# Performance work log

Hardware: AMD Instinct MI355X
Metric: run time of the kernel (lower is better)

Reference implementation:

```python
import jax, jax.numpy as jnp
import numpy as np

THR = 1.0
ALPHA = 5.0
C = 0.4
TAU_U = 20.0
DT = 1.0

def slayer(x):
    # SE-adlif SLAYER surrogate: c*alpha / (2*exp(alpha*|x|))
    return C * ALPHA / (2.0 * jnp.exp(jnp.abs(x) * ALPHA))

def setup_inputs() -> dict:
    key = jax.random.key(0)
    k1, k2, k3 = jax.random.split(key, 3)
    B, T, IN, OUT = 64, 1000, 512, 512
    x = jax.random.normal(k1, (B, T, IN), dtype=jnp.float32)
    lim = 1.0 / np.sqrt(IN)
    weight = jax.random.uniform(k2, (OUT, IN), minval=-lim, maxval=lim, dtype=jnp.float32)
    bias = jnp.zeros((OUT,), jnp.float32)
    # orthogonal init for recurrent weights
    recurrent = jnp.linalg.qr(jax.random.normal(k3, (OUT, OUT), dtype=jnp.float32))[0].astype(jnp.float32)
    # fixed tau trainer: decay = exp(-dt/tau)
    decay = jnp.full((OUT,), np.exp(-DT / TAU_U), dtype=jnp.float32)
    return {"input_tensor": x, "weight": weight, "bias": bias, "recurrent": recurrent, "decay": decay}

def reference(input_tensor, weight, bias, recurrent, decay):
    B = input_tensor.shape[0]
    OUT = weight.shape[0]
    sg = jax.lax.stop_gradient
    # precompute input-driven current for all timesteps: [B, T, OUT]
    cur = jnp.einsum('bti,oi->bto', input_tensor, weight) + bias
    v0 = jnp.zeros((B, OUT), jnp.float32)
    z0 = jnp.zeros((B, OUT), jnp.float32)

    def step(carry, c_t):
        v_tm1, z_tm1 = carry
        v_tm1 = v_tm1 * (1.0 - sg(z_tm1))  # detached reset
        soma = c_t + z_tm1 @ recurrent.T
        v_t = decay * v_tm1 + (1.0 - decay) * soma
        v_thr = v_t - THR
        hv = jnp.where(v_thr >= 0, 1.0, 0.0).astype(v_thr.dtype)
        # straight-through: value = heaviside, grad = SLAYER surrogate
        z_t = sg(hv) + (v_thr - sg(v_thr)) * sg(slayer(v_thr))
        return (v_t, z_t), (v_t, z_t)

    _, (vs, zs) = jax.lax.scan(step, (v0, z0), jnp.swapaxes(cur, 0, 1))
    vs = jnp.swapaxes(vs, 0, 1)  # [B, T, OUT]
    zs = jnp.swapaxes(zs, 0, 1)
    v_full = jnp.concatenate([v0[:, None], vs], axis=1)  # [B, T+1, OUT]
    z_full = jnp.concatenate([z0[:, None], zs], axis=1)
    states = jnp.stack([v_full, z_full], axis=0)  # [2, B, T+1, OUT]
    outputs = zs  # [B, T, OUT]
    return outputs, states
```

## Files before the change

kernel.cpp:

```cpp
#include <hip/hip_runtime.h>
#include <hip/hip_bf16.h>

#define SV_OFF 32768000
#define SZ_OFF 65568768
#define TC 125
#define NC 8

typedef __attribute__((ext_vector_type(8))) short bf16x8;
typedef __attribute__((ext_vector_type(4))) float f32x4;

__device__ __forceinline__ unsigned short f2bf(float f) {
  union { float f; unsigned u; } x; x.f = f;
  unsigned r = x.u + 0x7fffu + ((x.u >> 16) & 1u);
  return (unsigned short)(r >> 16);
}

__device__ __forceinline__ void gl_lds16(const void* g, void* l) {
  __builtin_amdgcn_global_load_lds(
      (const __attribute__((address_space(1))) unsigned int*)g,
      (__attribute__((address_space(3))) unsigned int*)l, 16, 0, 0);
}

__global__ __launch_bounds__(256) void prep(const float* __restrict__ W,
                                            const float* __restrict__ R,
                                            unsigned short* __restrict__ Wb,
                                            float* __restrict__ RT,
                                            int* __restrict__ flags) {
  const int idx = blockIdx.x * 256 + threadIdx.x;
  if (idx < 512 * 512) {
    Wb[idx] = f2bf(W[idx]);
    const int j = idx >> 9;
    const int o = idx & 511;
    RT[idx] = R[o * 512 + j];
  }
  if (idx < 64) flags[idx] = 0;
}

__global__ __launch_bounds__(256, 2) void gemm_cur(
    const float* __restrict__ A,
    const unsigned short* __restrict__ Wb,
    const float* __restrict__ bias,
    float* __restrict__ C) {
  __shared__ unsigned short As[128][40];
  __shared__ unsigned short Bs[128][32];
  const int tid = threadIdx.x;
  const int bn = blockIdx.x * 128;
  const int bm = blockIdx.y * 128;
  const int wave = tid >> 6;
  const int lane = tid & 63;
  const int lr = lane & 15;
  const int lq = lane >> 4;
  const int mh = (wave & 1) * 64;
  const int nh = (wave >> 1) * 64;

  f32x4 acc[4][4] = {};

  const int arow = tid >> 3;
  const int acol = (tid & 7) * 4;
  const int ldsoff0 = tid * 16;

  for (int kk = 0; kk < 16; ++kk) {
    const int k0 = kk * 32;
    __syncthreads();
#pragma unroll
    for (int p = 0; p < 4; ++p) {
      const int r = arow + p * 32;
      const float4 a4 = *(const float4*)(A + (size_t)(bm + r) * 512 + k0 + acol);
      ushort4 h;
      h.x = f2bf(a4.x); h.y = f2bf(a4.y); h.z = f2bf(a4.z); h.w = f2bf(a4.w);
      *(ushort4*)(&As[r][acol]) = h;
    }
#pragma unroll
    for (int q = 0; q < 2; ++q) {
      const int lo = q * 4096 + ldsoff0;
      const int row = lo >> 6;
      const int kb = lo & 63;
      gl_lds16((const char*)Wb + (size_t)(bn + row) * 1024 + (size_t)k0 * 2 + kb,
               (char*)(&Bs[0][0]) + lo);
    }
    __syncthreads();
    bf16x8 af[4], bfr[4];
#pragma unroll
    for (int i = 0; i < 4; ++i)
      af[i] = *(const bf16x8*)(&As[mh + i * 16 + lr][lq * 8]);
#pragma unroll
    for (int j = 0; j < 4; ++j)
      bfr[j] = *(const bf16x8*)(&Bs[nh + j * 16 + lr][lq * 8]);
#pragma unroll
    for (int i = 0; i < 4; ++i)
#pragma unroll
      for (int j = 0; j < 4; ++j)
        acc[i][j] = __builtin_amdgcn_mfma_f32_16x16x32_bf16(af[i], bfr[j], acc[i][j], 0, 0, 0);
  }
#pragma unroll
  for (int j = 0; j < 4; ++j) {
    const int col = bn + nh + j * 16 + lr;
    const float bv = bias[col];
#pragma unroll
    for (int i = 0; i < 4; ++i) {
      const int r0 = bm + mh + i * 16 + lq * 4;
#pragma unroll
      for (int r = 0; r < 4; ++r)
        C[(size_t)(r0 + r) * 512 + col] = acc[i][j][r] + bv;
    }
  }
}

__global__ __launch_bounds__(256) void chunk_sums(const float* __restrict__ cur,
                                                  const float* __restrict__ decay,
                                                  float* __restrict__ S) {
  const int gt = blockIdx.x * 256 + threadIdx.x;
  const int o = gt & 511;
  const int j = (gt >> 9) & (NC - 1);
  const int b = gt >> 12;
  const float d = decay[o];
  const float om = 1.0f - d;
  const size_t base = (size_t)b * 512000 + (size_t)(j * TC) * 512 + o;
  float nb[8];
#pragma unroll
  for (int u = 0; u < 8; ++u) nb[u] = cur[base + (size_t)u * 512];
  float s = 0.f;
#pragma unroll 8
  for (int k = 0; k < TC; ++k) {
    const float c = nb[k & 7];
    if (k < TC - 8) nb[k & 7] = cur[base + (size_t)(k + 8) * 512];
    s = d * s + om * c;
  }
  S[gt] = s;
}

__global__ __launch_bounds__(256) void chunk_prefix(const float* __restrict__ S,
                                                    const float* __restrict__ decay,
                                                    float* __restrict__ Vs) {
  const int gt = blockIdx.x * 256 + threadIdx.x;
  const int o = gt & 511;
  const int b = gt >> 9;
  const float d = decay[o];
  const float dTC = powf(d, (float)TC);
  float v = 0.f;
  const int base = (b << 12) + o;
#pragma unroll
  for (int j = 0; j < NC; ++j) {
    Vs[base + (j << 9)] = v;
    v = dTC * v + S[base + (j << 9)];
  }
}

__global__ __launch_bounds__(256) void chunk_scan(const float* __restrict__ cur,
                                                  const float* __restrict__ decay,
                                                  const float* __restrict__ Vs,
                                                  float* __restrict__ out,
                                                  int* __restrict__ flags) {
  const int gt = blockIdx.x * 256 + threadIdx.x;
  const int o = gt & 511;
  const int j = (gt >> 9) & (NC - 1);
  const int b = gt >> 12;
  const float d = decay[o];
  const float om = 1.0f - d;
  const size_t ci = (size_t)b * 512000 + (size_t)(j * TC) * 512 + o;
  const size_t svb = (size_t)b * 512512 + (size_t)(j * TC) * 512 + o;
  float* __restrict__ sv = out + SV_OFF;
  float* __restrict__ sz = out + SZ_OFF;
  if (j == 0) {
    __builtin_nontemporal_store(0.f, &sv[svb]);
    __builtin_nontemporal_store(0.f, &sz[svb]);
  }
  float v = Vs[(b << 12) + (j << 9) + o];
  int fl = 0;
  float nb[8];
#pragma unroll
  for (int u = 0; u < 8; ++u) nb[u] = cur[ci + (size_t)u * 512];
#pragma unroll 8
  for (int k = 0; k < TC; ++k) {
    const float c = nb[k & 7];
    if (k < TC - 8) nb[k & 7] = cur[ci + (size_t)(k + 8) * 512];
    v = d * v + om * c;
    const float z = (v >= 1.0f) ? 1.0f : 0.0f;
    fl |= (v >= 1.0f);
    const size_t row = (size_t)k * 512;
    __builtin_nontemporal_store(z, &out[ci + row]);
    __builtin_nontemporal_store(v, &sv[svb + row + 512]);
    __builtin_nontemporal_store(z, &sz[svb + row + 512]);
  }
  if (fl) atomicOr(flags + b, 1);
}

__global__ __launch_bounds__(512) void scan_fix(const float* __restrict__ cur,
                                                const float* __restrict__ decay,
                                                const float* __restrict__ RT,
                                                float* __restrict__ out,
                                                const int* __restrict__ flags) {
  const int b = blockIdx.x;
  if (flags[b] == 0) return;
  const int o = threadIdx.x;
  __shared__ int cnt;
  __shared__ int list[512];
  const float d = decay[o];
  const float om = 1.f - d;
  float v = 0.f, z = 0.f;
  const size_t ci = (size_t)b * 512000 + o;
  const size_t svb = (size_t)b * 512512 + o;
  float* __restrict__ sv = out + SV_OFF;
  float* __restrict__ sz = out + SZ_OFF;
  sv[svb] = 0.f;
  sz[svb] = 0.f;
  if (o == 0) cnt = 0;
  __syncthreads();
  for (int t = 0; t < 1000; ++t) {
    float soma = cur[ci + (size_t)t * 512];
    const int n = cnt;
    for (int i = 0; i < n; ++i) soma += RT[(size_t)list[i] * 512 + o];
    v = d * (v * (1.f - z)) + om * soma;
    z = (v >= 1.0f) ? 1.0f : 0.0f;
    out[ci + (size_t)t * 512] = z;
    sv[svb + (size_t)(t + 1) * 512] = v;
    sz[svb + (size_t)(t + 1) * 512] = z;
    __syncthreads();
    if (o == 0) cnt = 0;
    __syncthreads();
    if (z != 0.f) { const int p = atomicAdd(&cnt, 1); list[p] = o; }
    __syncthreads();
  }
}

extern "C" void kernel_launch(void* const* d_in, const int* in_sizes, int n_in,
                              void* d_out, int out_size, void* d_ws, size_t ws_size,
                              hipStream_t stream) {
  (void)in_sizes; (void)n_in; (void)out_size; (void)ws_size;
  const float* x     = (const float*)d_in[0];
  const float* W     = (const float*)d_in[1];
  const float* bias  = (const float*)d_in[2];
  const float* R     = (const float*)d_in[3];
  const float* decay = (const float*)d_in[4];
  float* out = (float*)d_out;

  char* ws = (char*)d_ws;
  float* cur          = (float*)ws;
  unsigned short* Wb  = (unsigned short*)(ws + 131072000);
  float* RT           = (float*)(ws + 131596288);
  int* flags          = (int*)(ws + 132644864);
  float* S            = (float*)(ws + 132648960);
  float* Vs           = (float*)(ws + 133697536);

  prep<<<1024, 256, 0, stream>>>(W, R, Wb, RT, flags);
  gemm_cur<<<dim3(4, 500), 256, 0, stream>>>(x, Wb, bias, cur);
  chunk_sums<<<1024, 256, 0, stream>>>(cur, decay, S);
  chunk_prefix<<<128, 256, 0, stream>>>(S, decay, Vs);
  chunk_scan<<<1024, 256, 0, stream>>>(cur, decay, Vs, out, flags);
  scan_fix<<<64, 512, 0, stream>>>(cur, decay, RT, out, flags);
}
```

Measured before the change: 619.9 us.

## Pre-convert input to bf16 and fold chunk prefix into chunk scan

Adds a separate pass that converts x to bf16 into the not-yet-written region of the output buffer. The GEMM then streams both operands straight into LDS with global_load_lds instead of converting fp32 in registers, and it reads half the bytes per tile, at the cost of an extra full read/write pass over x. It also removes the chunk_prefix kernel: each chunk_scan thread recomputes its starting state from the chunk sums, which saves a launch but adds a few redundant serial FMAs.

```diff
diff --git a/kernel.cpp b/kernel.cpp
--- a/kernel.cpp
+++ b/kernel.cpp
@@ -36,12 +36,25 @@
   if (idx < 64) flags[idx] = 0;
 }
 
+__global__ __launch_bounds__(256) void cvt_x(const float* __restrict__ x,
+                                             unsigned short* __restrict__ xb) {
+  const size_t i = ((size_t)blockIdx.x * 256 + threadIdx.x) * 8;
+  const float4 a = *(const float4*)(x + i);
+  const float4 b = *(const float4*)(x + i + 4);
+  bf16x8 h;
+  h[0] = (short)f2bf(a.x); h[1] = (short)f2bf(a.y);
+  h[2] = (short)f2bf(a.z); h[3] = (short)f2bf(a.w);
+  h[4] = (short)f2bf(b.x); h[5] = (short)f2bf(b.y);
+  h[6] = (short)f2bf(b.z); h[7] = (short)f2bf(b.w);
+  *(bf16x8*)(xb + i) = h;
+}
+
 __global__ __launch_bounds__(256, 2) void gemm_cur(
-    const float* __restrict__ A,
+    const unsigned short* __restrict__ Ab,
     const unsigned short* __restrict__ Wb,
     const float* __restrict__ bias,
     float* __restrict__ C) {
-  __shared__ unsigned short As[128][40];
+  __shared__ unsigned short As[128][32];
   __shared__ unsigned short Bs[128][32];
   const int tid = threadIdx.x;
   const int bn = blockIdx.x * 128;
@@ -55,29 +68,19 @@
 
   f32x4 acc[4][4] = {};
 
-  const int arow = tid >> 3;
-  const int acol = (tid & 7) * 4;
-  const int ldsoff0 = tid * 16;
+  const int lo0 = tid * 16;
+  const int row0 = lo0 >> 6;
+  const int colb = lo0 & 63;
+  const size_t abase = (size_t)(bm + row0) * 1024 + colb;
+  const size_t bbase = (size_t)(bn + row0) * 1024 + colb;
 
   for (int kk = 0; kk < 16; ++kk) {
-    const int k0 = kk * 32;
-    __syncthreads();
-#pragma unroll
-    for (int p = 0; p < 4; ++p) {
-      const int r = arow + p * 32;
-      const float4 a4 = *(const float4*)(A + (size_t)(bm + r) * 512 + k0 + acol);
-      ushort4 h;
-      h.x = f2bf(a4.x); h.y = f2bf(a4.y); h.z = f2bf(a4.z); h.w = f2bf(a4.w);
-      *(ushort4*)(&As[r][acol]) = h;
-    }
-#pragma unroll
-    for (int q = 0; q < 2; ++q) {
-      const int lo = q * 4096 + ldsoff0;
-      const int row = lo >> 6;
-      const int kb = lo & 63;
-      gl_lds16((const char*)Wb + (size_t)(bn + row) * 1024 + (size_t)k0 * 2 + kb,
-               (char*)(&Bs[0][0]) + lo);
-    }
+    const size_t koff = (size_t)kk * 64;
+    __syncthreads();
+    gl_lds16((const char*)Ab + abase + koff,            (char*)(&As[0][0]) + lo0);
+    gl_lds16((const char*)Ab + abase + 65536 + koff,    (char*)(&As[0][0]) + lo0 + 4096);
+    gl_lds16((const char*)Wb + bbase + koff,            (char*)(&Bs[0][0]) + lo0);
+    gl_lds16((const char*)Wb + bbase + 65536 + koff,    (char*)(&Bs[0][0]) + lo0 + 4096);
     __syncthreads();
     bf16x8 af[4], bfr[4];
 #pragma unroll
@@ -129,26 +132,9 @@
   S[gt] = s;
 }
 
-__global__ __launch_bounds__(256) void chunk_prefix(const float* __restrict__ S,
-                                                    const float* __restrict__ decay,
-                                                    float* __restrict__ Vs) {
-  const int gt = blockIdx.x * 256 + threadIdx.x;
-  const int o = gt & 511;
-  const int b = gt >> 9;
-  const float d = decay[o];
-  const float dTC = powf(d, (float)TC);
-  float v = 0.f;
-  const int base = (b << 12) + o;
-#pragma unroll
-  for (int j = 0; j < NC; ++j) {
-    Vs[base + (j << 9)] = v;
-    v = dTC * v + S[base + (j << 9)];
-  }
-}
-
 __global__ __launch_bounds__(256) void chunk_scan(const float* __restrict__ cur,
                                                   const float* __restrict__ decay,
-                                                  const float* __restrict__ Vs,
+                                                  const float* __restrict__ S,
                                                   float* __restrict__ out,
                                                   int* __restrict__ flags) {
   const int gt = blockIdx.x * 256 + threadIdx.x;
@@ -165,7 +151,12 @@
     __builtin_nontemporal_store(0.f, &sv[svb]);
     __builtin_nontemporal_store(0.f, &sz[svb]);
   }
-  float v = Vs[(b << 12) + (j << 9) + o];
+  float v = 0.f;
+  if (j > 0) {
+    const float dTC = powf(d, (float)TC);
+    const int sb = (b << 12) + o;
+    for (int jj = 0; jj < j; ++jj) v = dTC * v + S[sb + (jj << 9)];
+  }
   int fl = 0;
   float nb[8];
 #pragma unroll
@@ -240,12 +231,13 @@
   float* RT           = (float*)(ws + 131596288);
   int* flags          = (int*)(ws + 132644864);
   float* S            = (float*)(ws + 132648960);
-  float* Vs           = (float*)(ws + 133697536);
+
+  unsigned short* xb = (unsigned short*)(out + SV_OFF);
 
   prep<<<1024, 256, 0, stream>>>(W, R, Wb, RT, flags);
-  gemm_cur<<<dim3(4, 500), 256, 0, stream>>>(x, Wb, bias, cur);
+  cvt_x<<<16000, 256, 0, stream>>>(x, xb);
+  gemm_cur<<<dim3(4, 500), 256, 0, stream>>>(xb, Wb, bias, cur);
   chunk_sums<<<1024, 256, 0, stream>>>(cur, decay, S);
-  chunk_prefix<<<128, 256, 0, stream>>>(S, decay, Vs);
-  chunk_scan<<<1024, 256, 0, stream>>>(cur, decay, Vs, out, flags);
+  chunk_scan<<<1024, 256, 0, stream>>>(cur, decay, S, out, flags);
   scan_fix<<<64, 512, 0, stream>>>(cur, decay, RT, out, flags);
 }
```

New measurement: 603.3 us. -2.7%, faster.
